# Kernel tuning notes

Hardware: AMD Instinct MI355X
Metric: run time of the kernel (lower is better)

The kernel has to match this reference:

```python
import jax, jax.numpy as jnp
import numpy as np

N_NODES = 100000
N_EDGES = 800000
HIDDEN = 128


def setup_inputs() -> dict:
    key = jax.random.key(0)
    k1, k2, k3, k4, k5, k6 = jax.random.split(key, 6)
    z = jax.random.normal(k1, (N_NODES, HIDDEN), dtype=jnp.float32)
    edge_index = jax.random.randint(k2, (2, N_EDGES), 0, N_NODES, dtype=jnp.int64)
    # nn.Linear params (torch default init scale ~ 1/sqrt(fan_in))
    s1 = 1.0 / np.sqrt(2 * HIDDEN)
    s2 = 1.0 / np.sqrt(HIDDEN)
    W1 = jax.random.uniform(k3, (2 * HIDDEN, HIDDEN), jnp.float32, -s1, s1)
    b1 = jax.random.uniform(k4, (HIDDEN,), jnp.float32, -s1, s1)
    W2 = jax.random.uniform(k5, (HIDDEN, 1), jnp.float32, -s2, s2)
    b2 = jax.random.uniform(k6, (1,), jnp.float32, -s2, s2)
    return {"z": z, "edge_index": edge_index, "W1": W1, "b1": b1, "W2": W2, "b2": b2}


def reference(z, edge_index, W1, b1, W2, b2):
    src, dst = edge_index[0], edge_index[1]
    # Gather endpoint features: [E, H] each. Avoid materializing the [E, 2H]
    # concat by splitting W1 into src/dst halves (same math as cat + matmul).
    W1_src, W1_dst = W1[:HIDDEN], W1[HIDDEN:]
    h = z[src] @ W1_src + z[dst] @ W1_dst + b1  # [E, H]
    h = jax.nn.relu(h)
    score = h @ W2 + b2  # [E, 1]
    return score
```

## Files before the change

### kernel.cpp

```cpp
#include <hip/hip_runtime.h>
#include <hip/hip_bf16.h>

#define N_NODES 100000
#define N_EDGES 800000
#define HIDDEN 128
#define N_TILES 1563
#define PC_GRID 768

typedef short frag_ab __attribute__((ext_vector_type(8)));
typedef float frag_cd __attribute__((ext_vector_type(4)));

__device__ inline unsigned short f2b(float f) {
    union { float f; unsigned u; } x; x.f = f;
    return (unsigned short)((x.u + 0x7fffu + ((x.u >> 16) & 1u)) >> 16);
}

__device__ inline unsigned pk2(float x, float y) {
    union { __hip_bfloat162 h; unsigned u; } c;
    c.h = __float22bfloat162_rn(make_float2(x, y));
    return c.u;
}

__global__ __launch_bounds__(256) void transpose_w1(
    const float* __restrict__ W1, unsigned short* __restrict__ Bt)
{
    const int t  = threadIdx.x;
    const int nc = blockIdx.x * 4 + (t >> 6);
    const int k2 = (t & 63) * 2;
    const int col  = nc & 127;
    const int roff = (nc >= 128) ? 128 : 0;
    float f0 = W1[(size_t)(roff + k2)     * HIDDEN + col];
    float f1 = W1[(size_t)(roff + k2 + 1) * HIDDEN + col];
    *(unsigned*)(Bt + (size_t)nc * HIDDEN + k2) = (unsigned)f2b(f0) | ((unsigned)f2b(f1) << 16);
}

#define AS_STRIDE 136
#define CS_STRIDE 264

__global__ __launch_bounds__(256) void precompute_uv_mfma(
    const float* __restrict__ z, const unsigned short* __restrict__ Bt,
    const float* __restrict__ b1, unsigned short* __restrict__ UV)
{
    __shared__ unsigned short smem[64 * CS_STRIDE];
    const int t = threadIdx.x;
    const int lane = t & 63;
    const int w = t >> 6;
    const int wn = w * 64;
    const int g  = lane >> 4;
    const int lc = lane & 15;

    frag_ab b[4][4];
    float bias[4];
    #pragma unroll
    for (int nt = 0; nt < 4; ++nt) {
        int nc = wn + nt * 16 + lc;
        bias[nt] = (nc < HIDDEN) ? b1[nc] : 0.f;
        const unsigned short* brow = Bt + (size_t)nc * HIDDEN;
        #pragma unroll
        for (int q = 0; q < 4; ++q)
            b[nt][q] = *(const frag_ab*)(brow + q * 32 + g * 8);
    }

    int tile = blockIdx.x;
    uint2 pf[8];
    #pragma unroll
    for (int i = 0; i < 8; ++i) {
        int f4 = i * 256 + t;
        int m = tile * 64 + (f4 >> 5);
        if (m >= N_NODES) m = N_NODES - 1;
        float4 v = ((const float4*)z)[(size_t)m * 32 + (f4 & 31)];
        pf[i].x = pk2(v.x, v.y);
        pf[i].y = pk2(v.z, v.w);
    }

    while (true) {
        #pragma unroll
        for (int i = 0; i < 8; ++i) {
            int f4 = i * 256 + t;
            *(uint2*)&smem[(f4 >> 5) * AS_STRIDE + (f4 & 31) * 4] = pf[i];
        }
        __syncthreads();

        const int next = tile + PC_GRID;
        const bool have_next = (next < N_TILES);
        if (have_next) {
            #pragma unroll
            for (int i = 0; i < 8; ++i) {
                int f4 = i * 256 + t;
                int m = next * 64 + (f4 >> 5);
                if (m >= N_NODES) m = N_NODES - 1;
                float4 v = ((const float4*)z)[(size_t)m * 32 + (f4 & 31)];
                pf[i].x = pk2(v.x, v.y);
                pf[i].y = pk2(v.z, v.w);
            }
        }

        frag_cd acc[4][4];
        #pragma unroll
        for (int mt = 0; mt < 4; ++mt)
            #pragma unroll
            for (int nt = 0; nt < 4; ++nt)
                acc[mt][nt] = (frag_cd){0.f, 0.f, 0.f, 0.f};
        #pragma unroll
        for (int q = 0; q < 4; ++q) {
            frag_ab a[4];
            #pragma unroll
            for (int mt = 0; mt < 4; ++mt)
                a[mt] = *(const frag_ab*)&smem[(mt * 16 + lc) * AS_STRIDE + q * 32 + g * 8];
            #pragma unroll
            for (int mt = 0; mt < 4; ++mt)
                #pragma unroll
                for (int nt = 0; nt < 4; ++nt)
                    acc[mt][nt] = __builtin_amdgcn_mfma_f32_16x16x32_bf16(
                        a[mt], b[nt][q], acc[mt][nt], 0, 0, 0);
        }
        __syncthreads();

        #pragma unroll
        for (int nt = 0; nt < 4; ++nt) {
            int nc = wn + nt * 16 + lc;
            #pragma unroll
            for (int mt = 0; mt < 4; ++mt)
                #pragma unroll
                for (int r = 0; r < 4; ++r)
                    smem[(mt * 16 + g * 4 + r) * CS_STRIDE + nc] =
                        f2b(acc[mt][nt][r] + bias[nt]);
        }
        __syncthreads();

        const int m0 = tile * 64;
        #pragma unroll
        for (int i = 0; i < 8; ++i) {
            int f = i * 256 + t;
            int m = f >> 5;
            int c16 = f & 31;
            if (m0 + m < N_NODES) {
                uint4 val = *(const uint4*)&smem[m * CS_STRIDE + c16 * 8];
                *(uint4*)&UV[(size_t)(m0 + m) * 256 + c16 * 8] = val;
            }
        }
        if (!have_next) break;
        __syncthreads();
        tile = next;
    }
}

__device__ inline float2 bf2(unsigned u) {
    union { unsigned i; float f; } lo, hi;
    lo.i = u << 16;
    hi.i = u & 0xffff0000u;
    return make_float2(lo.f, hi.f);
}

__device__ inline float2 rfma2(unsigned u, unsigned v, float2 w, float2 acc) {
    float2 uf = bf2(u), vf = bf2(v);
    float2 s = make_float2(uf.x + vf.x, uf.y + vf.y);
    s.x = fmaxf(s.x, 0.f); s.y = fmaxf(s.y, 0.f);
    acc.x = __builtin_fmaf(s.x, w.x, acc.x);
    acc.y = __builtin_fmaf(s.y, w.y, acc.y);
    return acc;
}

__global__ __launch_bounds__(256) void edge_score(
    const int* __restrict__ ei, const unsigned short* __restrict__ UV,
    const float* __restrict__ W2, const float* __restrict__ B2,
    float* __restrict__ out)
{
    const int t = threadIdx.x;
    const int g = t & 7;
    const int slot = t >> 3;
    const int e0 = blockIdx.x * 64 + slot;
    const int e1 = e0 + 32;

    const float4* W24 = (const float4*)W2;
    const float4 w0 = W24[g * 4 + 0];
    const float4 w1 = W24[g * 4 + 1];
    const float4 w2 = W24[g * 4 + 2];
    const float4 w3 = W24[g * 4 + 3];

    const int s0 = ei[e0];
    const int d0 = ei[N_EDGES + e0];
    const int s1 = ei[e1];
    const int d1 = ei[N_EDGES + e1];

    const uint4* u0p = (const uint4*)(UV + (size_t)s0 * 256) + g * 2;
    const uint4* v0p = (const uint4*)(UV + (size_t)d0 * 256 + 128) + g * 2;
    const uint4* u1p = (const uint4*)(UV + (size_t)s1 * 256) + g * 2;
    const uint4* v1p = (const uint4*)(UV + (size_t)d1 * 256 + 128) + g * 2;
    const uint4 ua0 = u0p[0], ub0 = u0p[1];
    const uint4 va0 = v0p[0], vb0 = v0p[1];
    const uint4 ua1 = u1p[0], ub1 = u1p[1];
    const uint4 va1 = v1p[0], vb1 = v1p[1];

    float2 A = make_float2(0.f, 0.f), B = make_float2(0.f, 0.f);
    A = rfma2(ua0.x, va0.x, make_float2(w0.x, w0.y), A);
    A = rfma2(ua0.y, va0.y, make_float2(w0.z, w0.w), A);
    A = rfma2(ua0.z, va0.z, make_float2(w1.x, w1.y), A);
    A = rfma2(ua0.w, va0.w, make_float2(w1.z, w1.w), A);
    A = rfma2(ub0.x, vb0.x, make_float2(w2.x, w2.y), A);
    A = rfma2(ub0.y, vb0.y, make_float2(w2.z, w2.w), A);
    A = rfma2(ub0.z, vb0.z, make_float2(w3.x, w3.y), A);
    A = rfma2(ub0.w, vb0.w, make_float2(w3.z, w3.w), A);

    B = rfma2(ua1.x, va1.x, make_float2(w0.x, w0.y), B);
    B = rfma2(ua1.y, va1.y, make_float2(w0.z, w0.w), B);
    B = rfma2(ua1.z, va1.z, make_float2(w1.x, w1.y), B);
    B = rfma2(ua1.w, va1.w, make_float2(w1.z, w1.w), B);
    B = rfma2(ub1.x, vb1.x, make_float2(w2.x, w2.y), B);
    B = rfma2(ub1.y, vb1.y, make_float2(w2.z, w2.w), B);
    B = rfma2(ub1.z, vb1.z, make_float2(w3.x, w3.y), B);
    B = rfma2(ub1.w, vb1.w, make_float2(w3.z, w3.w), B);

    float sa = A.x + A.y;
    float sb = B.x + B.y;
    sa += __shfl_xor(sa, 1, 8);
    sa += __shfl_xor(sa, 2, 8);
    sa += __shfl_xor(sa, 4, 8);
    sb += __shfl_xor(sb, 1, 8);
    sb += __shfl_xor(sb, 2, 8);
    sb += __shfl_xor(sb, 4, 8);

    if (g == 0) {
        float bb = B2[0];
        out[e0] = sa + bb;
        out[e1] = sb + bb;
    }
}

extern "C" void kernel_launch(void* const* d_in, const int* in_sizes, int n_in,
                              void* d_out, int out_size, void* d_ws, size_t ws_size,
                              hipStream_t stream) {
    const float* z  = (const float*)d_in[0];
    const int*   ei = (const int*)d_in[1];
    const float* W1 = (const float*)d_in[2];
    const float* b1 = (const float*)d_in[3];
    const float* W2 = (const float*)d_in[4];
    const float* b2 = (const float*)d_in[5];
    float* out = (float*)d_out;

    unsigned short* UV = (unsigned short*)d_ws;
    unsigned short* Bt = UV + (size_t)N_NODES * 256;

    transpose_w1<<<64, 256, 0, stream>>>(W1, Bt);
    precompute_uv_mfma<<<PC_GRID, 256, 0, stream>>>(z, Bt, b1, UV);
    edge_score<<<N_EDGES / 64, 256, 0, stream>>>(ei, UV, W2, b2, out);
}
```

Measured before the change: 166.6 us.

## Restructure UV precompute: one tile per block, A in registers, B streamed

Replaces the persistent, prefetching precompute kernel with a non-persistent launch of one 64-node tile per block. Each wave now handles 16 rows across all 256 output columns. The A fragments are loaded straight from global z into registers, skipping the shared-memory staging, and the W1 fragments are streamed from global memory per column tile. This removes the block-wide barriers and the A-tile shared-memory pass. In exchange it loses the cross-tile load prefetch, and every wave rereads the whole B matrix from cache.

```diff
diff --git a/kernel.cpp b/kernel.cpp
--- a/kernel.cpp
+++ b/kernel.cpp
@@ -4,8 +4,6 @@
 #define N_NODES 100000
 #define N_EDGES 800000
 #define HIDDEN 128
-#define N_TILES 1563
-#define PC_GRID 768
 
 typedef short frag_ab __attribute__((ext_vector_type(8)));
 typedef float frag_cd __attribute__((ext_vector_type(4)));
@@ -34,114 +32,74 @@
     *(unsigned*)(Bt + (size_t)nc * HIDDEN + k2) = (unsigned)f2b(f0) | ((unsigned)f2b(f1) << 16);
 }
 
-#define AS_STRIDE 136
 #define CS_STRIDE 264
 
 __global__ __launch_bounds__(256) void precompute_uv_mfma(
     const float* __restrict__ z, const unsigned short* __restrict__ Bt,
     const float* __restrict__ b1, unsigned short* __restrict__ UV)
 {
-    __shared__ unsigned short smem[64 * CS_STRIDE];
+    __shared__ unsigned short Cs[64 * CS_STRIDE];
     const int t = threadIdx.x;
     const int lane = t & 63;
     const int w = t >> 6;
-    const int wn = w * 64;
     const int g  = lane >> 4;
     const int lc = lane & 15;
-
-    frag_ab b[4][4];
-    float bias[4];
-    #pragma unroll
-    for (int nt = 0; nt < 4; ++nt) {
-        int nc = wn + nt * 16 + lc;
-        bias[nt] = (nc < HIDDEN) ? b1[nc] : 0.f;
-        const unsigned short* brow = Bt + (size_t)nc * HIDDEN;
-        #pragma unroll
-        for (int q = 0; q < 4; ++q)
-            b[nt][q] = *(const frag_ab*)(brow + q * 32 + g * 8);
-    }
-
-    int tile = blockIdx.x;
-    uint2 pf[8];
-    #pragma unroll
-    for (int i = 0; i < 8; ++i) {
-        int f4 = i * 256 + t;
-        int m = tile * 64 + (f4 >> 5);
-        if (m >= N_NODES) m = N_NODES - 1;
-        float4 v = ((const float4*)z)[(size_t)m * 32 + (f4 & 31)];
-        pf[i].x = pk2(v.x, v.y);
-        pf[i].y = pk2(v.z, v.w);
-    }
-
-    while (true) {
-        #pragma unroll
-        for (int i = 0; i < 8; ++i) {
-            int f4 = i * 256 + t;
-            *(uint2*)&smem[(f4 >> 5) * AS_STRIDE + (f4 & 31) * 4] = pf[i];
-        }
-        __syncthreads();
-
-        const int next = tile + PC_GRID;
-        const bool have_next = (next < N_TILES);
-        if (have_next) {
-            #pragma unroll
-            for (int i = 0; i < 8; ++i) {
-                int f4 = i * 256 + t;
-                int m = next * 64 + (f4 >> 5);
-                if (m >= N_NODES) m = N_NODES - 1;
-                float4 v = ((const float4*)z)[(size_t)m * 32 + (f4 & 31)];
-                pf[i].x = pk2(v.x, v.y);
-                pf[i].y = pk2(v.z, v.w);
-            }
-        }
-
-        frag_cd acc[4][4];
-        #pragma unroll
-        for (int mt = 0; mt < 4; ++mt)
-            #pragma unroll
-            for (int nt = 0; nt < 4; ++nt)
-                acc[mt][nt] = (frag_cd){0.f, 0.f, 0.f, 0.f};
+    const int m0 = blockIdx.x * 64 + w * 16;
+
+    frag_ab a[4];
+    {
+        int mr = m0 + lc; if (mr > N_NODES - 1) mr = N_NODES - 1;
+        const float4* zr = (const float4*)(z + (size_t)mr * HIDDEN);
         #pragma unroll
         for (int q = 0; q < 4; ++q) {
-            frag_ab a[4];
-            #pragma unroll
-            for (int mt = 0; mt < 4; ++mt)
-                a[mt] = *(const frag_ab*)&smem[(mt * 16 + lc) * AS_STRIDE + q * 32 + g * 8];
-            #pragma unroll
-            for (int mt = 0; mt < 4; ++mt)
-                #pragma unroll
-                for (int nt = 0; nt < 4; ++nt)
-                    acc[mt][nt] = __builtin_amdgcn_mfma_f32_16x16x32_bf16(
-                        a[mt], b[nt][q], acc[mt][nt], 0, 0, 0);
+            float4 v0 = zr[q * 8 + g * 2];
+            float4 v1 = zr[q * 8 + g * 2 + 1];
+            union { frag_ab f; unsigned u[4]; } c;
+            c.u[0] = pk2(v0.x, v0.y);
+            c.u[1] = pk2(v0.z, v0.w);
+            c.u[2] = pk2(v1.x, v1.y);
+            c.u[3] = pk2(v1.z, v1.w);
+            a[q] = c.f;
         }
-        __syncthreads();
-
+    }
+
+    frag_cd acc[16];
+    #pragma unroll
+    for (int nt = 0; nt < 16; ++nt)
+        acc[nt] = (frag_cd){0.f, 0.f, 0.f, 0.f};
+
+    #pragma unroll
+    for (int nt = 0; nt < 16; ++nt) {
+        const unsigned short* brow = Bt + (size_t)(nt * 16 + lc) * HIDDEN + g * 8;
+        frag_ab b0 = *(const frag_ab*)(brow);
+        frag_ab bq1 = *(const frag_ab*)(brow + 32);
+        frag_ab bq2 = *(const frag_ab*)(brow + 64);
+        frag_ab bq3 = *(const frag_ab*)(brow + 96);
+        acc[nt] = __builtin_amdgcn_mfma_f32_16x16x32_bf16(a[0], b0,  acc[nt], 0, 0, 0);
+        acc[nt] = __builtin_amdgcn_mfma_f32_16x16x32_bf16(a[1], bq1, acc[nt], 0, 0, 0);
+        acc[nt] = __builtin_amdgcn_mfma_f32_16x16x32_bf16(a[2], bq2, acc[nt], 0, 0, 0);
+        acc[nt] = __builtin_amdgcn_mfma_f32_16x16x32_bf16(a[3], bq3, acc[nt], 0, 0, 0);
+    }
+
+    #pragma unroll
+    for (int nt = 0; nt < 16; ++nt) {
+        int nc = nt * 16 + lc;
+        float bias = (nc < HIDDEN) ? b1[nc] : 0.f;
         #pragma unroll
-        for (int nt = 0; nt < 4; ++nt) {
-            int nc = wn + nt * 16 + lc;
-            #pragma unroll
-            for (int mt = 0; mt < 4; ++mt)
-                #pragma unroll
-                for (int r = 0; r < 4; ++r)
-                    smem[(mt * 16 + g * 4 + r) * CS_STRIDE + nc] =
-                        f2b(acc[mt][nt][r] + bias[nt]);
+        for (int r = 0; r < 4; ++r)
+            Cs[(w * 16 + g * 4 + r) * CS_STRIDE + nc] = f2b(acc[nt][r] + bias);
+    }
+
+    #pragma unroll
+    for (int i = 0; i < 8; ++i) {
+        int idx = i * 64 + lane;
+        int row = idx >> 5;
+        int c16 = idx & 31;
+        int m = m0 + row;
+        if (m < N_NODES) {
+            uint4 val = *(const uint4*)&Cs[(w * 16 + row) * CS_STRIDE + c16 * 8];
+            *(uint4*)&UV[(size_t)m * 256 + c16 * 8] = val;
         }
-        __syncthreads();
-
-        const int m0 = tile * 64;
-        #pragma unroll
-        for (int i = 0; i < 8; ++i) {
-            int f = i * 256 + t;
-            int m = f >> 5;
-            int c16 = f & 31;
-            if (m0 + m < N_NODES) {
-                uint4 val = *(const uint4*)&smem[m * CS_STRIDE + c16 * 8];
-                *(uint4*)&UV[(size_t)(m0 + m) * 256 + c16 * 8] = val;
-            }
-        }
-        if (!have_next) break;
-        __syncthreads();
-        tile = next;
     }
 }
 
@@ -242,6 +200,6 @@
     unsigned short* Bt = UV + (size_t)N_NODES * 256;
 
     transpose_w1<<<64, 256, 0, stream>>>(W1, Bt);
-    precompute_uv_mfma<<<PC_GRID, 256, 0, stream>>>(z, Bt, b1, UV);
+    precompute_uv_mfma<<<(N_NODES + 63) / 64, 256, 0, stream>>>(z, Bt, b1, UV);
     edge_score<<<N_EDGES / 64, 256, 0, stream>>>(ei, UV, W2, b2, out);
 }
```

After: 213.2 us. +28.0%, slower.
